# Performance work log

Hardware: AMD Instinct MI355X
Metric: run time of the kernel (lower is better)

Reference implementation:

```python
import jax, jax.numpy as jnp
import numpy as np

D_MODEL = 256
KSIZE = 16
EPS = 1e-5


def conv1d(x, w, b):
    # x: [B, C, N], w: [O, C, K], SAME padding over node axis
    y = jax.lax.conv_general_dilated(x, w, window_strides=(1,), padding='SAME',
                                     dimension_numbers=('NCH', 'OIH', 'NCH'))
    return y + b[None, :, None]


def layernorm(x, g, b):
    mu = jnp.mean(x, axis=-1, keepdims=True)
    var = jnp.mean(jnp.square(x - mu), axis=-1, keepdims=True)
    return (x - mu) * jax.lax.rsqrt(var + EPS) * g + b


def setup_inputs() -> dict:
    key = jax.random.key(0)
    ks = jax.random.split(key, 16)
    B, N, d, K = 4, 2048, D_MODEL, KSIZE
    conv_scale = 1.0 / np.sqrt(d * K)
    lin_scale = 1.0 / np.sqrt(d)
    return {
        'src': jax.random.normal(ks[0], (B, N, d), jnp.float32),
        'x_lst': jnp.zeros((B, N, N), jnp.float32),
        'adj': jax.random.randint(ks[1], (B, N, N), 0, 2, jnp.int32),
        'dis': jax.random.uniform(ks[2], (B, N, N), jnp.float32),
        'Wq': jax.random.normal(ks[3], (d, d, K), jnp.float32) * conv_scale,
        'bq': jnp.zeros((d,), jnp.float32),
        'Wk': jax.random.normal(ks[4], (d, d, K), jnp.float32) * conv_scale,
        'bk': jnp.zeros((d,), jnp.float32),
        'Wv': jax.random.normal(ks[5], (d, d, K), jnp.float32) * conv_scale,
        'bv': jnp.zeros((d,), jnp.float32),
        'W1': jax.random.normal(ks[6], (d, d), jnp.float32) * lin_scale,
        'b1': jnp.zeros((d,), jnp.float32),
        'W2': jax.random.normal(ks[7], (d, d), jnp.float32) * lin_scale,
        'b2': jnp.zeros((d,), jnp.float32),
        'W3': jax.random.normal(ks[8], (d, d), jnp.float32) * lin_scale,
        'b3': jnp.zeros((d,), jnp.float32),
        'g1': jnp.ones((d,), jnp.float32),
        'be1': jnp.zeros((d,), jnp.float32),
        'g2': jnp.ones((d,), jnp.float32),
        'be2': jnp.zeros((d,), jnp.float32),
    }


def reference(src, x_lst, adj, dis, Wq, bq, Wk, bk, Wv, bv,
              W1, b1, W2, b2, W3, b3, g1, be1, g2, be2):
    # ---- _ga_block: transpose to channel-major, graph attention ----
    x = jnp.swapaxes(src, -2, -1)                      # [B, d, N]
    q = conv1d(x, Wq, bq)                              # [B, d, N]
    k = conv1d(x, Wk, bk)
    v = conv1d(x, Wv, bv)
    scale = 1.0 / jnp.sqrt(jnp.asarray(D_MODEL, src.dtype))
    scores = jnp.einsum('bdn,bdm->bnm', q, k) * scale  # [B, N, N]
    scores = scores - dis                              # distance bias
    scores = jnp.where(adj > 0, scores, jnp.asarray(-1e9, scores.dtype))
    attn = jax.nn.softmax(scores, axis=-1)             # [B, N, N]
    x_lst_new = x_lst + attn                           # accumulated attention state
    out = jnp.einsum('bnm,bdm->bdn', attn, v)          # [B, d, N]
    x1 = jnp.swapaxes(out, -2, -1)                     # [B, N, d] (dropout = identity in eval)
    # ---- residual + norm1 ----
    h = layernorm(src + x1, g1, be1)
    # ---- 3-layer LeakyReLU MLP + residual + norm2 ----
    m = jax.nn.leaky_relu(h @ W1.T + b1)
    m = jax.nn.leaky_relu(m @ W2.T + b2)
    m = m @ W3.T + b3
    h = layernorm(h + m, g2, be2)
    return h, x_lst_new
```

## Files before the change

kernel.cpp:

```cpp
#include <hip/hip_runtime.h>
#include <stdint.h>

typedef _Float16 h16;
typedef _Float16 h4v __attribute__((ext_vector_type(4)));
typedef _Float16 h8v __attribute__((ext_vector_type(8)));
typedef float    f4v __attribute__((ext_vector_type(4)));
typedef int      i4v __attribute__((ext_vector_type(4)));

#define NBATCH 4
#define NNODE  2048
#define DM     256
#define NPAD   2063
#define QKELEM 2097152
#define PARTN  (8192 * 256)

__device__ __forceinline__ void async16(const void* g, void* l) {
#if __has_builtin(__builtin_amdgcn_global_load_lds)
  __builtin_amdgcn_global_load_lds((__attribute__((address_space(1))) void*)g,
                                   (__attribute__((address_space(3))) void*)l, 16, 0, 0);
#else
  *(f4v*)l = *(const f4v*)g;
#endif
}

#define BARRIER() do { asm volatile("" ::: "memory"); __builtin_amdgcn_s_barrier(); asm volatile("" ::: "memory"); } while (0)
#define MFMA16 __builtin_amdgcn_mfma_f32_16x16x32_f16

__device__ __forceinline__ void gemm_tile(
    const h16* Abase, int astride,
    const h16* Bbase, int bstride,
    h16* As, h16* Bs, f4v acc[4][4], int kiters)
{
  const int tid  = threadIdx.x;
  const int lane = tid & 63;
  const int wv   = tid >> 6;
  const int srow = tid >> 2;
  const int sch  = ((tid & 3) ^ ((tid >> 3) & 3)) * 8;
  const h16* gA0 = Abase + (long)srow * astride + sch;
  const h16* gA1 = Abase + (long)(srow + 64) * astride + sch;
  const h16* gB0 = Bbase + (long)srow * bstride + sch;
  const h16* gB1 = Bbase + (long)(srow + 64) * bstride + sch;
  h16* lA0 = As + tid * 8;
  h16* lA1 = As + 2048 + tid * 8;
  h16* lB0 = Bs + tid * 8;
  h16* lB1 = Bs + 2048 + tid * 8;
  const int swz = ((lane & 15) >> 1) & 3;
  const int qq  = ((lane >> 4) ^ swz) * 8;
  const int amr = ((wv & 1) * 64 + (lane & 15)) * 32 + qq;
  const int bnr = ((wv >> 1) * 64 + (lane & 15)) * 32 + qq;

  for (int kt = 0; kt < kiters; ++kt) {
    const int k0 = kt * 32;
    __syncthreads();
    async16(gA0 + k0, lA0);
    async16(gA1 + k0, lA1);
    async16(gB0 + k0, lB0);
    async16(gB1 + k0, lB1);
    asm volatile("s_waitcnt vmcnt(0)" ::: "memory");
    __syncthreads();
    h8v af[4], bf[4];
#pragma unroll
    for (int i = 0; i < 4; ++i) af[i] = *(const h8v*)(As + amr + i * 512);
#pragma unroll
    for (int j = 0; j < 4; ++j) bf[j] = *(const h8v*)(Bs + bnr + j * 512);
#pragma unroll
    for (int i = 0; i < 4; ++i)
#pragma unroll
      for (int j = 0; j < 4; ++j)
        acc[i][j] = MFMA16(af[i], bf[j], acc[i][j], 0, 0, 0);
  }
}

__device__ __forceinline__ void zero_acc(f4v acc[4][4]) {
#pragma unroll
  for (int i = 0; i < 4; ++i)
#pragma unroll
    for (int j = 0; j < 4; ++j) {
      f4v z = {0.f, 0.f, 0.f, 0.f};
      acc[i][j] = z;
    }
}

template<int ASTRIDE, int BSTRIDE>
__device__ __forceinline__ void gemm256_pipe(
    const h16* __restrict__ Abase, const h16* __restrict__ Bbase,
    h16* As, h16* Bs, f4v (&acc)[8][4], const int kiters)
{
  const int tid  = threadIdx.x;
  const int lane = tid & 63, wv = tid >> 6;

  const int rh = tid >> 3;
  const int cs = (((tid & 7) ^ ((tid >> 3) & 7)) << 3);
  const h16* AgT = Abase + (long)rh * ASTRIDE + cs;
  const h16* BgT = Bbase + (long)rh * BSTRIDE + cs;
  h16* lA = As + tid * 8;
  h16* lB = Bs + tid * 8;

  auto stageA = [&](int kt, int half) {
    h16* d = lA + ((kt & 1) << 14) + (half << 13);
    const h16* g = AgT + (long)half * 128 * ASTRIDE + kt * 64;
    async16(g, d);
    async16(g + 64 * ASTRIDE, d + 4096);
  };
  auto stageB = [&](int kt, int half) {
    h16* d = lB + ((kt & 1) << 14) + (half << 13);
    const h16* g = BgT + (long)half * 128 * BSTRIDE + kt * 64;
    async16(g, d);
    async16(g + 64 * BSTRIDE, d + 4096);
  };

  const int wr = wv >> 2, wc = wv & 3;
  const int e0 = (((lane >> 4) ^ (lane & 7)) << 3);
  const int e1 = e0 ^ 32;
  const h16* pA0 = As + (wr * 128 + (lane & 15)) * 64 + e0;
  const h16* pA1 = pA0 + (e1 - e0);
  const h16* pB0 = Bs + (wc * 64 + (lane & 15)) * 64 + e0;
  const h16* pB1 = pB0 + (e1 - e0);

#pragma unroll
  for (int i = 0; i < 8; ++i)
#pragma unroll
    for (int j = 0; j < 4; ++j) { f4v z = {0.f, 0.f, 0.f, 0.f}; acc[i][j] = z; }

  stageA(0, 0); stageA(0, 1); stageB(0, 0); stageB(0, 1); stageA(1, 0);
  asm volatile("s_waitcnt vmcnt(2)" ::: "memory");
  BARRIER();

#pragma unroll 1
  for (int kt = 0; kt < kiters; ++kt) {
    const int sb = (kt & 1) << 14;
    h8v ar[4][2], bL[2][2], bR[2][2];
#pragma unroll
    for (int i = 0; i < 4; ++i) {
      ar[i][0] = *(const h8v*)(pA0 + sb + i * 1024);
      ar[i][1] = *(const h8v*)(pA1 + sb + i * 1024);
    }
#pragma unroll
    for (int j = 0; j < 2; ++j) {
      bL[j][0] = *(const h8v*)(pB0 + sb + j * 1024);
      bL[j][1] = *(const h8v*)(pB1 + sb + j * 1024);
    }
    if (kt < kiters - 1) stageA(kt + 1, 1);
    BARRIER();
    __builtin_amdgcn_s_setprio(1);
#pragma unroll
    for (int i = 0; i < 4; ++i)
#pragma unroll
      for (int j = 0; j < 2; ++j) {
        acc[i][j] = MFMA16(ar[i][0], bL[j][0], acc[i][j], 0, 0, 0);
        acc[i][j] = MFMA16(ar[i][1], bL[j][1], acc[i][j], 0, 0, 0);
      }
    __builtin_amdgcn_s_setprio(0);
    BARRIER();
#pragma unroll
    for (int j = 0; j < 2; ++j) {
      bR[j][0] = *(const h8v*)(pB0 + sb + (j + 2) * 1024);
      bR[j][1] = *(const h8v*)(pB1 + sb + (j + 2) * 1024);
    }
    if (kt < kiters - 1) stageB(kt + 1, 0);
    BARRIER();
    __builtin_amdgcn_s_setprio(1);
#pragma unroll
    for (int i = 0; i < 4; ++i)
#pragma unroll
      for (int j = 0; j < 2; ++j) {
        acc[i][j + 2] = MFMA16(ar[i][0], bR[j][0], acc[i][j + 2], 0, 0, 0);
        acc[i][j + 2] = MFMA16(ar[i][1], bR[j][1], acc[i][j + 2], 0, 0, 0);
      }
    __builtin_amdgcn_s_setprio(0);
    BARRIER();
#pragma unroll
    for (int i = 0; i < 4; ++i) {
      ar[i][0] = *(const h8v*)(pA0 + sb + (i + 4) * 1024);
      ar[i][1] = *(const h8v*)(pA1 + sb + (i + 4) * 1024);
    }
    if (kt < kiters - 1) stageB(kt + 1, 1);
    BARRIER();
    __builtin_amdgcn_s_setprio(1);
#pragma unroll
    for (int i = 0; i < 4; ++i)
#pragma unroll
      for (int j = 0; j < 2; ++j) {
        acc[i + 4][j + 2] = MFMA16(ar[i][0], bR[j][0], acc[i + 4][j + 2], 0, 0, 0);
        acc[i + 4][j + 2] = MFMA16(ar[i][1], bR[j][1], acc[i + 4][j + 2], 0, 0, 0);
      }
    __builtin_amdgcn_s_setprio(0);
    BARRIER();
#pragma unroll
    for (int j = 0; j < 2; ++j) {
      bL[j][0] = *(const h8v*)(pB0 + sb + j * 1024);
      bL[j][1] = *(const h8v*)(pB1 + sb + j * 1024);
    }
    if (kt < kiters - 2) {
      stageA(kt + 2, 0);
      asm volatile("s_waitcnt vmcnt(2)" ::: "memory");
    } else if (kt == kiters - 2) {
      asm volatile("s_waitcnt vmcnt(0)" ::: "memory");
    }
    BARRIER();
    __builtin_amdgcn_s_setprio(1);
#pragma unroll
    for (int i = 0; i < 4; ++i)
#pragma unroll
      for (int j = 0; j < 2; ++j) {
        acc[i + 4][j] = MFMA16(ar[i][0], bL[j][0], acc[i + 4][j], 0, 0, 0);
        acc[i + 4][j] = MFMA16(ar[i][1], bL[j][1], acc[i + 4][j], 0, 0, 0);
      }
    __builtin_amdgcn_s_setprio(0);
    BARRIER();
  }
}

#define NSRC_BLK 8252
__global__ __launch_bounds__(256) void prep_all_kernel(
    const float* __restrict__ src,
    const float* __restrict__ Wq, const float* __restrict__ Wk, const float* __restrict__ Wv,
    const float* __restrict__ W1, const float* __restrict__ W2, const float* __restrict__ W3,
    h16* __restrict__ Xpad, h16* __restrict__ Wt, h16* __restrict__ Wl)
{
  __shared__ float plds[16][257];
  const int bi = blockIdx.x, tid = threadIdx.x;
  if (bi < NSRC_BLK) {
    int idx = bi * 256 + tid;
    int c = idx & 255;
    int row = idx >> 8;
    int b = row / NPAD;
    int n = row - b * NPAD;
    float v = 0.f;
    int ns = n - 7;
    if (ns >= 0 && ns < NNODE) v = src[((long)b * NNODE + ns) * DM + c];
    Xpad[idx] = (h16)v;
  } else if (bi < NSRC_BLK + 768) {
    const int q = bi - NSRC_BLK;
    const int w = q >> 8, o = q & 255;
    const float* W = (w == 0) ? Wq : (w == 1) ? Wk : Wv;
    const float* base = W + (long)o * 4096;
    f4v r0 = *(const f4v*)(base + tid * 16);
    f4v r1 = *(const f4v*)(base + tid * 16 + 4);
    f4v r2 = *(const f4v*)(base + tid * 16 + 8);
    f4v r3 = *(const f4v*)(base + tid * 16 + 12);
#pragma unroll
    for (int k = 0; k < 4; ++k) {
      plds[k][tid] = r0[k]; plds[4 + k][tid] = r1[k];
      plds[8 + k][tid] = r2[k]; plds[12 + k][tid] = r3[k];
    }
    __syncthreads();
    const int t = tid >> 4, c0 = (tid & 15) * 16;
    h16* out = Wt + ((long)(w * 256 + o)) * 4096 + t * 256 + c0;
    h8v o0, o1;
#pragma unroll
    for (int k = 0; k < 8; ++k) { o0[k] = (h16)plds[t][c0 + k]; o1[k] = (h16)plds[t][c0 + 8 + k]; }
    *(h8v*)out = o0;
    *(h8v*)(out + 8) = o1;
  } else {
    int idx = (bi - NSRC_BLK - 768) * 256 + tid;
    int w = idx >> 16;
    int rem = idx & 65535;
    const float* W = (w == 0) ? W1 : (w == 1) ? W2 : W3;
    Wl[idx] = (h16)W[rem];
  }
}

__global__ __launch_bounds__(512) void conv_gemm256_kernel(
    const h16* __restrict__ Xpad, const h16* __restrict__ Wt,
    h16* __restrict__ Qp, h16* __restrict__ Kp, h16* __restrict__ Vp)
{
  __shared__ __align__(16) h16 As[32768];
  __shared__ __align__(16) h16 Bs[32768];
  const int lane = threadIdx.x & 63, wv = threadIdx.x >> 6;
  const int mt = blockIdx.x, w = blockIdx.y, ks = blockIdx.z;
  const int m0 = mt * 256;
  const int b  = m0 >> 11, n0 = m0 & 2047;

  const h16* Abase = Xpad + ((long)(b * NPAD + n0) << 8) + ((long)ks << 11);
  const h16* Bbase = Wt + ((long)w << 20) + ((long)ks << 11);

  f4v acc[8][4];
  gemm256_pipe<256, 4096>(Abase, Bbase, As, Bs, acc, 32);

  h16* dst = ((w == 0) ? Qp : (w == 1) ? Kp : Vp) + (long)ks * QKELEM;
  const int wr = wv >> 2, wc = wv & 3;
  const int rb = (lane >> 4) * 4;
  const int cb = wc * 64 + (lane & 15);
  const int mrow0 = m0 + wr * 128;
#pragma unroll
  for (int i = 0; i < 8; ++i)
#pragma unroll
    for (int j = 0; j < 4; ++j) {
      const int gc = cb + j * 16;
#pragma unroll
      for (int e = 0; e < 4; ++e) {
        const int gr = mrow0 + i * 16 + rb + e;
        dst[(long)gr * 256 + gc] = (h16)acc[i][j][e];
      }
    }
}

__global__ __launch_bounds__(256) void conv_reduce_kernel(
    const h16* __restrict__ Qp, const h16* __restrict__ Kp, const h16* __restrict__ Vp,
    const float* __restrict__ bq, const float* __restrict__ bk, const float* __restrict__ bv,
    h16* __restrict__ Qb, h16* __restrict__ Kb, h16* __restrict__ Vt)
{
  __shared__ float T[64][65];
  const int bi = blockIdx.x, tid = threadIdx.x;
  if (bi < 2048) {
    const long gid = (long)bi * 256 + tid;
    const int which = gid >= (QKELEM / 8);
    const long e = (gid - (long)which * (QKELEM / 8)) * 8;
    const h16* P = which ? Kp : Qp;
    const float* bias = which ? bk : bq;
    h8v p0 = *(const h8v*)(P + e);
    h8v p1 = *(const h8v*)(P + QKELEM + e);
    const int c0 = (int)(e & 255);
    h8v o;
#pragma unroll
    for (int k = 0; k < 8; ++k) o[k] = (h16)((float)p0[k] + (float)p1[k] + bias[c0 + k]);
    *(h8v*)((which ? Kb : Qb) + e) = o;
  } else {
    const int q = bi - 2048;
    const int mt = q >> 2, ct = q & 3;
    const int m0 = mt * 64, c0 = ct * 64;
    const int b = m0 >> 11, n0 = m0 & 2047;
    const int rr = tid >> 3, cc = (tid & 7) * 8;
#pragma unroll
    for (int p = 0; p < 2; ++p) {
      const int r = p * 32 + rr;
      const long so = (long)(m0 + r) * 256 + c0 + cc;
      h8v p0 = *(const h8v*)(Vp + so);
      h8v p1 = *(const h8v*)(Vp + QKELEM + so);
#pragma unroll
      for (int e = 0; e < 8; ++e) T[r][cc + e] = (float)p0[e] + (float)p1[e];
    }
    __syncthreads();
#pragma unroll
    for (int p = 0; p < 2; ++p) {
      const int d = p * 32 + rr;
      const float bias_v = bv[c0 + d];
      h8v o;
#pragma unroll
      for (int e = 0; e < 8; ++e) o[e] = (h16)(T[cc + e][d] + bias_v);
      *(h8v*)(Vt + ((long)(b * 256 + c0 + d)) * 2048 + n0 + cc) = o;
    }
  }
}

#define MBS 144
__global__ __launch_bounds__(256) void scores_gemm_kernel(
    const h16* __restrict__ Q, const h16* __restrict__ Km,
    const float* __restrict__ dis, const int* __restrict__ adj,
    h16* __restrict__ Sh)
{
  __shared__ __align__(16) h16 As[4096];
  __shared__ __align__(16) h16 Bs[4096];
  __shared__ __align__(16) h16 Mb[128 * MBS];
  const int nt = blockIdx.x, mt = blockIdx.y, b = blockIdx.z;
  const int tid = threadIdx.x, lane = tid & 63, wv = tid >> 6;

  const h16* Abase = Q + ((long)b * NNODE + nt * 128) * 256;
  const h16* Bbase = Km + ((long)b * NNODE + mt * 128) * 256;

  const int srow = tid >> 2;
  const int sch  = ((tid & 3) ^ ((tid >> 3) & 3)) * 8;
  const h16* gA0 = Abase + (long)srow * 256 + sch;
  const h16* gA1 = Abase + (long)(srow + 64) * 256 + sch;
  const h16* gB0 = Bbase + (long)srow * 256 + sch;
  const h16* gB1 = Bbase + (long)(srow + 64) * 256 + sch;
  h16* lA0 = As + tid * 8;
  h16* lA1 = As + 2048 + tid * 8;
  h16* lB0 = Bs + tid * 8;
  h16* lB1 = Bs + 2048 + tid * 8;
  const int swz = ((lane & 15) >> 1) & 3;
  const int qq  = ((lane >> 4) ^ swz) * 8;
  const int amr = ((wv & 1) * 64 + (lane & 15)) * 32 + qq;
  const int bnr = ((wv >> 1) * 64 + (lane & 15)) * 32 + qq;

  const long gbase = (long)b * NNODE * NNODE + (long)(nt * 128) * 2048 + mt * 128;
  f4v acc[4][4];
  zero_acc(acc);

#pragma unroll 1
  for (int kt = 0; kt < 8; ++kt) {
    const int f0 = kt * 2048 + tid * 4;
    const int f1 = f0 + 1024;
    const int r0 = f0 >> 7, c0 = f0 & 127;
    const int r1 = f1 >> 7, c1 = f1 & 127;
    const long g0 = gbase + (long)r0 * 2048 + c0;
    const long g1 = gbase + (long)r1 * 2048 + c1;
    __syncthreads();
    f4v dv0 = *(const f4v*)(dis + g0);
    f4v dv1 = *(const f4v*)(dis + g1);
    i4v av0 = *(const i4v*)(adj + g0);
    i4v av1 = *(const i4v*)(adj + g1);
    const int k0 = kt * 32;
    async16(gA0 + k0, lA0);
    async16(gA1 + k0, lA1);
    async16(gB0 + k0, lB0);
    async16(gB1 + k0, lB1);
    asm volatile("s_waitcnt vmcnt(0)" ::: "memory");
    h4v m0, m1;
#pragma unroll
    for (int k = 0; k < 4; ++k) {
      m0[k] = (av0[k] > 0) ? (h16)(-dv0[k]) : (h16)(-30000.0f);
      m1[k] = (av1[k] > 0) ? (h16)(-dv1[k]) : (h16)(-30000.0f);
    }
    *(h4v*)(Mb + r0 * MBS + c0) = m0;
    *(h4v*)(Mb + r1 * MBS + c1) = m1;
    __syncthreads();
    h8v af[4], bf[4];
#pragma unroll
    for (int i = 0; i < 4; ++i) af[i] = *(const h8v*)(As + amr + i * 512);
#pragma unroll
    for (int j = 0; j < 4; ++j) bf[j] = *(const h8v*)(Bs + bnr + j * 512);
#pragma unroll
    for (int i = 0; i < 4; ++i)
#pragma unroll
      for (int j = 0; j < 4; ++j)
        acc[i][j] = MFMA16(af[i], bf[j], acc[i][j], 0, 0, 0);
  }

  const int rbase = (wv & 1) * 64 + (lane >> 4) * 4;
  const int cbase = (wv >> 1) * 64 + (lane & 15);
#pragma unroll
  for (int i = 0; i < 4; ++i) {
#pragma unroll
    for (int e = 0; e < 4; ++e) {
      const int row = rbase + i * 16 + e;
      const long ro = gbase + (long)row * 2048;
#pragma unroll
      for (int j = 0; j < 4; ++j) {
        const int col = cbase + j * 16;
        const float sv = acc[i][j][e] * 0.0625f + (float)Mb[row * MBS + col];
        Sh[ro + col] = (h16)sv;
      }
    }
  }
}

__global__ __launch_bounds__(256) void softmax_kernel(
    h16* __restrict__ Sh, const float* __restrict__ x_lst, float* __restrict__ out_x)
{
  const int r = blockIdx.x;
  const long ro = (long)r * 2048;
  const int tid = threadIdx.x, lane = tid & 63, wv = tid >> 6;
  const int j0 = tid * 4;
  __shared__ float wmax[4], wsum[4];

  h4v sv0 = *(const h4v*)(Sh + ro + j0);
  h4v sv1 = *(const h4v*)(Sh + ro + 1024 + j0);

  float s[8];
#pragma unroll
  for (int k = 0; k < 4; ++k) { s[k] = (float)sv0[k]; s[k + 4] = (float)sv1[k]; }

  float m = s[0];
#pragma unroll
  for (int k = 1; k < 8; ++k) m = fmaxf(m, s[k]);
#pragma unroll
  for (int off = 32; off > 0; off >>= 1) m = fmaxf(m, __shfl_xor(m, off, 64));
  if (lane == 0) wmax[wv] = m;
  __syncthreads();
  m = fmaxf(fmaxf(wmax[0], wmax[1]), fmaxf(wmax[2], wmax[3]));

  float p[8], ls = 0.f;
#pragma unroll
  for (int k = 0; k < 8; ++k) { p[k] = __expf(s[k] - m); ls += p[k]; }
#pragma unroll
  for (int off = 32; off > 0; off >>= 1) ls += __shfl_xor(ls, off, 64);
  if (lane == 0) wsum[wv] = ls;
  __syncthreads();
  const float inv = 1.0f / (wsum[0] + wsum[1] + wsum[2] + wsum[3]);

  f4v x0 = *(const f4v*)(x_lst + ro + j0);
  f4v x1 = *(const f4v*)(x_lst + ro + 1024 + j0);
  f4v o0, o1;
  h4v pv0, pv1;
#pragma unroll
  for (int k = 0; k < 4; ++k) {
    const float a = p[k] * inv, bq = p[k + 4] * inv;
    o0[k] = x0[k] + a; o1[k] = x1[k] + bq;
    pv0[k] = (h16)a; pv1[k] = (h16)bq;
  }
  *(f4v*)(out_x + ro + j0) = o0;
  *(f4v*)(out_x + ro + 1024 + j0) = o1;
  *(h4v*)(Sh + ro + j0) = pv0;
  *(h4v*)(Sh + ro + 1024 + j0) = pv1;
}

__global__ __launch_bounds__(256) void av_gemm_kernel(
    const h16* __restrict__ Attn, const h16* __restrict__ Vt, h16* __restrict__ X1p)
{
  __shared__ __align__(16) h16 As[4096];
  __shared__ __align__(16) h16 Bs[4096];
  const int nt = blockIdx.x, b = blockIdx.z;
  const int ct = blockIdx.y & 1, ks = blockIdx.y >> 1;
  const h16* Abase = Attn + ((long)b * NNODE + nt * 128) * 2048 + ks * 1024;
  const h16* Bbase = Vt + ((long)b * 256 + ct * 128) * 2048 + ks * 1024;
  f4v acc[4][4];
  zero_acc(acc);
  gemm_tile(Abase, 2048, Bbase, 2048, As, Bs, acc, 32);

  const int lane = threadIdx.x & 63, wv = threadIdx.x >> 6;
  const int rbase = (wv & 1) * 64 + (lane >> 4) * 4;
  const int cbase = (wv >> 1) * 64 + (lane & 15);
  h16* dst = X1p + (long)ks * PARTN;
#pragma unroll
  for (int i = 0; i < 4; ++i) {
#pragma unroll
    for (int e = 0; e < 4; ++e) {
      const long row = (long)b * NNODE + nt * 128 + rbase + i * 16 + e;
#pragma unroll
      for (int j = 0; j < 4; ++j) {
        const int col = ct * 128 + cbase + j * 16;
        dst[row * 256 + col] = (h16)acc[i][j][e];
      }
    }
  }
}

__device__ __forceinline__ float wred_sum(float v) {
#pragma unroll
  for (int off = 32; off > 0; off >>= 1) v += __shfl_xor(v, off, 64);
  return v;
}

__global__ __launch_bounds__(256) void ln1_kernel(
    const float* __restrict__ X, const h16* __restrict__ Y, const h16* __restrict__ Y2,
    const float* __restrict__ g, const float* __restrict__ bb,
    float* __restrict__ outF, h16* __restrict__ outH)
{
  const int wv = threadIdx.x >> 6, lane = threadIdx.x & 63;
  const long r = (long)blockIdx.x * 4 + wv;
  const long off = r * 256 + lane * 4;
  f4v x = *(const f4v*)(X + off);
  h4v y = *(const h4v*)(Y + off);
  h4v y2 = *(const h4v*)(Y2 + off);
  float v[4];
  float sum = 0.f, sq = 0.f;
#pragma unroll
  for (int k = 0; k < 4; ++k) {
    v[k] = x[k] + (float)y[k] + (float)y2[k];
    sum += v[k]; sq += v[k] * v[k];
  }
  sum = wred_sum(sum);
  sq  = wred_sum(sq);
  const float mu = sum * (1.0f / 256.0f);
  const float var = sq * (1.0f / 256.0f) - mu * mu;
  const float rs = rsqrtf(var + 1e-5f);
  f4v gg = *(const f4v*)(g + lane * 4);
  f4v be = *(const f4v*)(bb + lane * 4);
  f4v o;
#pragma unroll
  for (int k = 0; k < 4; ++k) o[k] = (v[k] - mu) * rs * gg[k] + be[k];
  *(f4v*)(outF + off) = o;
  h4v hv;
#pragma unroll
  for (int k = 0; k < 4; ++k) hv[k] = (h16)o[k];
  *(h4v*)(outH + off) = hv;
}

__global__ __launch_bounds__(256) void mlp_fused_kernel(
    const h16* __restrict__ H16, const float* __restrict__ Hf,
    const h16* __restrict__ Wl,
    const float* __restrict__ b1, const float* __restrict__ b2, const float* __restrict__ b3,
    const float* __restrict__ g2, const float* __restrict__ be2,
    float* __restrict__ out_h)
{
  __shared__ h16 Xa[32][264];
  __shared__ h16 Xb[32][264];
  __shared__ __align__(16) h16 Bs[8192];
  const int tid = threadIdx.x, lane = tid & 63, wv = tid >> 6;
  const int m0 = blockIdx.x * 32;

  {
    const int r = tid >> 3, cq = (tid & 7) * 32;
    const h16* s = H16 + (long)(m0 + r) * 256 + cq;
#pragma unroll
    for (int k = 0; k < 4; ++k)
      *(h8v*)&Xa[r][cq + k * 8] = *(const h8v*)(s + k * 8);
  }

  const int srow = tid >> 2;
  const int sch  = ((tid & 3) ^ ((tid >> 3) & 3)) * 8;
  h16* lB = Bs + tid * 8;
  const int quad = lane >> 4;
  const float* biases[3] = {b1, b2, b3};

  for (int layer = 0; layer < 3; ++layer) {
    const h16* W = Wl + layer * 65536;
    const h16 (*Xi)[264] = (layer == 1) ? (const h16(*)[264])Xb : (const h16(*)[264])Xa;
    h16 (*Xo)[264] = (layer == 1) ? Xa : Xb;
    f4v acc[2][4];
#pragma unroll
    for (int i = 0; i < 2; ++i)
#pragma unroll
      for (int j = 0; j < 4; ++j) { f4v z = {0.f,0.f,0.f,0.f}; acc[i][j] = z; }

    for (int kt = 0; kt < 8; ++kt) {
      __syncthreads();
      const h16* gB = W + (long)srow * 256 + kt * 32 + sch;
      async16(gB, lB);
      async16(gB + 64 * 256, lB + 64 * 32);
      async16(gB + 128 * 256, lB + 128 * 32);
      async16(gB + 192 * 256, lB + 192 * 32);
      asm volatile("s_waitcnt vmcnt(0)" ::: "memory");
      __syncthreads();
      h8v af[2], bf[4];
#pragma unroll
      for (int i = 0; i < 2; ++i)
        af[i] = *(const h8v*)&Xi[i * 16 + (lane & 15)][kt * 32 + quad * 8];
#pragma unroll
      for (int j = 0; j < 4; ++j) {
        const int n = wv * 64 + j * 16 + (lane & 15);
        const int q = (quad ^ ((n >> 1) & 3)) * 8;
        bf[j] = *(const h8v*)(Bs + n * 32 + q);
      }
#pragma unroll
      for (int i = 0; i < 2; ++i)
#pragma unroll
        for (int j = 0; j < 4; ++j)
          acc[i][j] = MFMA16(af[i], bf[j], acc[i][j], 0, 0, 0);
    }
    const int rb = quad * 4;
    const int cb = wv * 64 + (lane & 15);
    const float* bias = biases[layer];
    const bool leaky = (layer < 2);
#pragma unroll
    for (int j = 0; j < 4; ++j) {
      const int col = cb + j * 16;
      const float bv = bias[col];
#pragma unroll
      for (int i = 0; i < 2; ++i)
#pragma unroll
        for (int e = 0; e < 4; ++e) {
          float v = acc[i][j][e] + bv;
          if (leaky) v = (v >= 0.f) ? v : 0.01f * v;
          Xo[i * 16 + rb + e][col] = (h16)v;
        }
    }
  }
  __syncthreads();

  const int r = tid >> 3, c0 = (tid & 7) * 32;
  const float* hrow = Hf + (long)(m0 + r) * 256 + c0;
  float v[32];
  float s = 0.f, sq = 0.f;
#pragma unroll
  for (int k8 = 0; k8 < 8; ++k8) {
    f4v h4 = *(const f4v*)(hrow + k8 * 4);
#pragma unroll
    for (int e = 0; e < 4; ++e) {
      float t = (float)Xb[r][c0 + k8 * 4 + e] + h4[e];
      v[k8 * 4 + e] = t; s += t; sq += t * t;
    }
  }
#pragma unroll
  for (int off = 1; off < 8; off <<= 1) { s += __shfl_xor(s, off, 64); sq += __shfl_xor(sq, off, 64); }
  const float mu = s * (1.0f / 256.0f);
  const float var = sq * (1.0f / 256.0f) - mu * mu;
  const float rs = rsqrtf(var + 1e-5f);
  float* orow = out_h + (long)(m0 + r) * 256 + c0;
#pragma unroll
  for (int k8 = 0; k8 < 8; ++k8) {
    f4v gg = *(const f4v*)(g2 + c0 + k8 * 4);
    f4v be = *(const f4v*)(be2 + c0 + k8 * 4);
    f4v o;
#pragma unroll
    for (int e = 0; e < 4; ++e) o[e] = (v[k8 * 4 + e] - mu) * rs * gg[e] + be[e];
    *(f4v*)(orow + k8 * 4) = o;
  }
}

extern "C" void kernel_launch(void* const* d_in, const int* in_sizes, int n_in,
                              void* d_out, int out_size, void* d_ws, size_t ws_size,
                              hipStream_t stream)
{
  const float* src  = (const float*)d_in[0];
  const float* xlst = (const float*)d_in[1];
  const int*   adj  = (const int*)d_in[2];
  const float* dis  = (const float*)d_in[3];
  const float* Wq   = (const float*)d_in[4];
  const float* bq   = (const float*)d_in[5];
  const float* Wk   = (const float*)d_in[6];
  const float* bk   = (const float*)d_in[7];
  const float* Wv   = (const float*)d_in[8];
  const float* bvp  = (const float*)d_in[9];
  const float* W1   = (const float*)d_in[10];
  const float* b1   = (const float*)d_in[11];
  const float* W2   = (const float*)d_in[12];
  const float* b2   = (const float*)d_in[13];
  const float* W3   = (const float*)d_in[14];
  const float* b3   = (const float*)d_in[15];
  const float* g1   = (const float*)d_in[16];
  const float* be1  = (const float*)d_in[17];
  const float* g2   = (const float*)d_in[18];
  const float* be2  = (const float*)d_in[19];
  (void)in_sizes; (void)n_in; (void)out_size; (void)ws_size;

  char* ws = (char*)d_ws;
  size_t off = 0;
  auto alloc = [&](size_t bytes) -> void* {
    void* p = ws + off;
    off += (bytes + 1023) & ~(size_t)1023;
    return p;
  };
  h16*   Xpad = (h16*)  alloc((size_t)NBATCH * NPAD * DM * 2);
  h16*   Wt   = (h16*)  alloc((size_t)3 * 256 * 4096 * 2);
  h16*   Wl   = (h16*)  alloc((size_t)3 * 256 * 256 * 2);
  h16*   Qb   = (h16*)  alloc((size_t)QKELEM * 2);
  h16*   Kb   = (h16*)  alloc((size_t)QKELEM * 2);
  h16*   Vt   = (h16*)  alloc((size_t)QKELEM * 2);
  char*  R    = (char*) alloc((size_t)66000 * 1024);
  h16*   Qp   = (h16*)R;
  h16*   Kp   = (h16*)(R + (size_t)2 * QKELEM * 2);
  h16*   Vp   = (h16*)(R + (size_t)4 * QKELEM * 2);
  h16*   Sh   = (h16*)R;
  h16*   X1p  = (h16*)(R + (size_t)8 * QKELEM * 2);
  float* H    = (float*)(R + (size_t)12 * QKELEM * 2);
  h16*   H16  = (h16*)((char*)H + (size_t)PARTN * 4);

  float* out_h = (float*)d_out;
  float* out_x = out_h + (size_t)NBATCH * NNODE * DM;

  prep_all_kernel<<<NSRC_BLK + 768 + 768, 256, 0, stream>>>(
      src, Wq, Wk, Wv, W1, W2, W3, Xpad, Wt, Wl);
  conv_gemm256_kernel<<<dim3(32, 3, 2), 512, 0, stream>>>(Xpad, Wt, Qp, Kp, Vp);
  conv_reduce_kernel<<<2048 + 512, 256, 0, stream>>>(
      Qp, Kp, Vp, bq, bk, bvp, Qb, Kb, Vt);
  scores_gemm_kernel<<<dim3(16, 16, 4), 256, 0, stream>>>(Qb, Kb, dis, adj, Sh);
  softmax_kernel<<<NBATCH * NNODE, 256, 0, stream>>>(Sh, xlst, out_x);
  av_gemm_kernel<<<dim3(16, 4, 4), 256, 0, stream>>>(Sh, Vt, X1p);
  ln1_kernel<<<(NBATCH * NNODE) / 4, 256, 0, stream>>>(src, X1p, X1p + PARTN, g1, be1, H, H16);
  mlp_fused_kernel<<<NBATCH * NNODE / 32, 256, 0, stream>>>(
      H16, H, Wl, b1, b2, b3, g2, be2, out_h);
}
```

Measured before the change: 413.1 us.

## Replace split-K conv GEMM with full-K 128x192 tiles and fused bias epilogue

```diff
diff --git a/kernel.cpp b/kernel.cpp
--- a/kernel.cpp
+++ b/kernel.cpp
@@ -79,136 +79,6 @@
       f4v z = {0.f, 0.f, 0.f, 0.f};
       acc[i][j] = z;
     }
-}
-
-template<int ASTRIDE, int BSTRIDE>
-__device__ __forceinline__ void gemm256_pipe(
-    const h16* __restrict__ Abase, const h16* __restrict__ Bbase,
-    h16* As, h16* Bs, f4v (&acc)[8][4], const int kiters)
-{
-  const int tid  = threadIdx.x;
-  const int lane = tid & 63, wv = tid >> 6;
-
-  const int rh = tid >> 3;
-  const int cs = (((tid & 7) ^ ((tid >> 3) & 7)) << 3);
-  const h16* AgT = Abase + (long)rh * ASTRIDE + cs;
-  const h16* BgT = Bbase + (long)rh * BSTRIDE + cs;
-  h16* lA = As + tid * 8;
-  h16* lB = Bs + tid * 8;
-
-  auto stageA = [&](int kt, int half) {
-    h16* d = lA + ((kt & 1) << 14) + (half << 13);
-    const h16* g = AgT + (long)half * 128 * ASTRIDE + kt * 64;
-    async16(g, d);
-    async16(g + 64 * ASTRIDE, d + 4096);
-  };
-  auto stageB = [&](int kt, int half) {
-    h16* d = lB + ((kt & 1) << 14) + (half << 13);
-    const h16* g = BgT + (long)half * 128 * BSTRIDE + kt * 64;
-    async16(g, d);
-    async16(g + 64 * BSTRIDE, d + 4096);
-  };
-
-  const int wr = wv >> 2, wc = wv & 3;
-  const int e0 = (((lane >> 4) ^ (lane & 7)) << 3);
-  const int e1 = e0 ^ 32;
-  const h16* pA0 = As + (wr * 128 + (lane & 15)) * 64 + e0;
-  const h16* pA1 = pA0 + (e1 - e0);
-  const h16* pB0 = Bs + (wc * 64 + (lane & 15)) * 64 + e0;
-  const h16* pB1 = pB0 + (e1 - e0);
-
-#pragma unroll
-  for (int i = 0; i < 8; ++i)
-#pragma unroll
-    for (int j = 0; j < 4; ++j) { f4v z = {0.f, 0.f, 0.f, 0.f}; acc[i][j] = z; }
-
-  stageA(0, 0); stageA(0, 1); stageB(0, 0); stageB(0, 1); stageA(1, 0);
-  asm volatile("s_waitcnt vmcnt(2)" ::: "memory");
-  BARRIER();
-
-#pragma unroll 1
-  for (int kt = 0; kt < kiters; ++kt) {
-    const int sb = (kt & 1) << 14;
-    h8v ar[4][2], bL[2][2], bR[2][2];
-#pragma unroll
-    for (int i = 0; i < 4; ++i) {
-      ar[i][0] = *(const h8v*)(pA0 + sb + i * 1024);
-      ar[i][1] = *(const h8v*)(pA1 + sb + i * 1024);
-    }
-#pragma unroll
-    for (int j = 0; j < 2; ++j) {
-      bL[j][0] = *(const h8v*)(pB0 + sb + j * 1024);
-      bL[j][1] = *(const h8v*)(pB1 + sb + j * 1024);
-    }
-    if (kt < kiters - 1) stageA(kt + 1, 1);
-    BARRIER();
-    __builtin_amdgcn_s_setprio(1);
-#pragma unroll
-    for (int i = 0; i < 4; ++i)
-#pragma unroll
-      for (int j = 0; j < 2; ++j) {
-        acc[i][j] = MFMA16(ar[i][0], bL[j][0], acc[i][j], 0, 0, 0);
-        acc[i][j] = MFMA16(ar[i][1], bL[j][1], acc[i][j], 0, 0, 0);
-      }
-    __builtin_amdgcn_s_setprio(0);
-    BARRIER();
-#pragma unroll
-    for (int j = 0; j < 2; ++j) {
-      bR[j][0] = *(const h8v*)(pB0 + sb + (j + 2) * 1024);
-      bR[j][1] = *(const h8v*)(pB1 + sb + (j + 2) * 1024);
-    }
-    if (kt < kiters - 1) stageB(kt + 1, 0);
-    BARRIER();
-    __builtin_amdgcn_s_setprio(1);
-#pragma unroll
-    for (int i = 0; i < 4; ++i)
-#pragma unroll
-      for (int j = 0; j < 2; ++j) {
-        acc[i][j + 2] = MFMA16(ar[i][0], bR[j][0], acc[i][j + 2], 0, 0, 0);
-        acc[i][j + 2] = MFMA16(ar[i][1], bR[j][1], acc[i][j + 2], 0, 0, 0);
-      }
-    __builtin_amdgcn_s_setprio(0);
-    BARRIER();
-#pragma unroll
-    for (int i = 0; i < 4; ++i) {
-      ar[i][0] = *(const h8v*)(pA0 + sb + (i + 4) * 1024);
-      ar[i][1] = *(const h8v*)(pA1 + sb + (i + 4) * 1024);
-    }
-    if (kt < kiters - 1) stageB(kt + 1, 1);
-    BARRIER();
-    __builtin_amdgcn_s_setprio(1);
-#pragma unroll
-    for (int i = 0; i < 4; ++i)
-#pragma unroll
-      for (int j = 0; j < 2; ++j) {
-        acc[i + 4][j + 2] = MFMA16(ar[i][0], bR[j][0], acc[i + 4][j + 2], 0, 0, 0);
-        acc[i + 4][j + 2] = MFMA16(ar[i][1], bR[j][1], acc[i + 4][j + 2], 0, 0, 0);
-      }
-    __builtin_amdgcn_s_setprio(0);
-    BARRIER();
-#pragma unroll
-    for (int j = 0; j < 2; ++j) {
-      bL[j][0] = *(const h8v*)(pB0 + sb + j * 1024);
-      bL[j][1] = *(const h8v*)(pB1 + sb + j * 1024);
-    }
-    if (kt < kiters - 2) {
-      stageA(kt + 2, 0);
-      asm volatile("s_waitcnt vmcnt(2)" ::: "memory");
-    } else if (kt == kiters - 2) {
-      asm volatile("s_waitcnt vmcnt(0)" ::: "memory");
-    }
-    BARRIER();
-    __builtin_amdgcn_s_setprio(1);
-#pragma unroll
-    for (int i = 0; i < 4; ++i)
-#pragma unroll
-      for (int j = 0; j < 2; ++j) {
-        acc[i + 4][j] = MFMA16(ar[i][0], bL[j][0], acc[i + 4][j], 0, 0, 0);
-        acc[i + 4][j] = MFMA16(ar[i][1], bL[j][1], acc[i + 4][j], 0, 0, 0);
-      }
-    __builtin_amdgcn_s_setprio(0);
-    BARRIER();
-  }
 }
 
 #define NSRC_BLK 8252
@@ -261,86 +131,139 @@
   }
 }
 
-__global__ __launch_bounds__(512) void conv_gemm256_kernel(
+__global__ __launch_bounds__(512) void conv_gemm_full(
     const h16* __restrict__ Xpad, const h16* __restrict__ Wt,
-    h16* __restrict__ Qp, h16* __restrict__ Kp, h16* __restrict__ Vp)
-{
-  __shared__ __align__(16) h16 As[32768];
-  __shared__ __align__(16) h16 Bs[32768];
-  const int lane = threadIdx.x & 63, wv = threadIdx.x >> 6;
-  const int mt = blockIdx.x, w = blockIdx.y, ks = blockIdx.z;
-  const int m0 = mt * 256;
-  const int b  = m0 >> 11, n0 = m0 & 2047;
-
-  const h16* Abase = Xpad + ((long)(b * NPAD + n0) << 8) + ((long)ks << 11);
-  const h16* Bbase = Wt + ((long)w << 20) + ((long)ks << 11);
-
-  f4v acc[8][4];
-  gemm256_pipe<256, 4096>(Abase, Bbase, As, Bs, acc, 32);
-
-  h16* dst = ((w == 0) ? Qp : (w == 1) ? Kp : Vp) + (long)ks * QKELEM;
+    const float* __restrict__ bq, const float* __restrict__ bk, const float* __restrict__ bv,
+    h16* __restrict__ Qb, h16* __restrict__ Kb, h16* __restrict__ Vp)
+{
+  __shared__ __align__(16) h16 As[16384];
+  __shared__ __align__(16) h16 Bs[24576];
+  const int tid = threadIdx.x, lane = tid & 63, wv = tid >> 6;
+  const int mt = blockIdx.x, nt = blockIdx.y;
+  const int m0 = mt * 128;
+  const int b = m0 >> 11, n0 = m0 & 2047;
+
+  const int rh = tid >> 3;
+  const int cs = (((tid & 7) ^ ((tid >> 3) & 7)) << 3);
+  const h16* AgT = Xpad + ((long)(b * NPAD + n0) << 8) + (long)rh * 256 + cs;
+  const h16* BgT = Wt + (long)(nt * 192) * 4096 + (long)rh * 4096 + cs;
+  h16* lA = As + tid * 8;
+  h16* lB = Bs + tid * 8;
+
+  auto stageA = [&](int kt, int half) {
+    async16(AgT + (long)half * (64 * 256) + kt * 64,
+            lA + ((kt & 1) << 13) + (half << 12));
+  };
+  auto stageB = [&](int kt, int third) {
+    async16(BgT + (long)third * (64 * 4096) + kt * 64,
+            lB + (kt & 1) * 12288 + third * 4096);
+  };
+
   const int wr = wv >> 2, wc = wv & 3;
-  const int rb = (lane >> 4) * 4;
-  const int cb = wc * 64 + (lane & 15);
-  const int mrow0 = m0 + wr * 128;
-#pragma unroll
-  for (int i = 0; i < 8; ++i)
-#pragma unroll
-    for (int j = 0; j < 4; ++j) {
-      const int gc = cb + j * 16;
+  const int e0 = (((lane >> 4) ^ (lane & 7)) << 3);
+  const int e1 = e0 ^ 32;
+  const h16* pA0 = As + (wr * 64 + (lane & 15)) * 64 + e0;
+  const h16* pA1 = As + (wr * 64 + (lane & 15)) * 64 + e1;
+  const h16* pB0 = Bs + (wc * 48 + (lane & 15)) * 64 + e0;
+  const h16* pB1 = Bs + (wc * 48 + (lane & 15)) * 64 + e1;
+
+  f4v acc[4][3];
+#pragma unroll
+  for (int i = 0; i < 4; ++i)
+#pragma unroll
+    for (int j = 0; j < 3; ++j) { f4v z = {0.f, 0.f, 0.f, 0.f}; acc[i][j] = z; }
+
+  stageA(0, 0); stageA(0, 1); stageB(0, 0); stageB(0, 1); stageB(0, 2); stageA(1, 0);
+  asm volatile("s_waitcnt vmcnt(1)" ::: "memory");
+  BARRIER();
+
+#pragma unroll 1
+  for (int kt = 0; kt < 64; ++kt) {
+    const int sa = (kt & 1) << 13;
+    const int sb = (kt & 1) * 12288;
+    h8v a0[4], a1[4], bL[2][2], b2[2];
+#pragma unroll
+    for (int i = 0; i < 4; ++i) {
+      a0[i] = *(const h8v*)(pA0 + sa + i * 1024);
+      a1[i] = *(const h8v*)(pA1 + sa + i * 1024);
+    }
+#pragma unroll
+    for (int j = 0; j < 2; ++j) {
+      bL[j][0] = *(const h8v*)(pB0 + sb + j * 1024);
+      bL[j][1] = *(const h8v*)(pB1 + sb + j * 1024);
+    }
+    if (kt < 63) stageA(kt + 1, 1);
+    BARRIER();
+    __builtin_amdgcn_s_setprio(1);
+#pragma unroll
+    for (int i = 0; i < 4; ++i)
+#pragma unroll
+      for (int j = 0; j < 2; ++j) {
+        acc[i][j] = MFMA16(a0[i], bL[j][0], acc[i][j], 0, 0, 0);
+        acc[i][j] = MFMA16(a1[i], bL[j][1], acc[i][j], 0, 0, 0);
+      }
+    __builtin_amdgcn_s_setprio(0);
+    BARRIER();
+    b2[0] = *(const h8v*)(pB0 + sb + 2 * 1024);
+    b2[1] = *(const h8v*)(pB1 + sb + 2 * 1024);
+    if (kt < 63) { stageB(kt + 1, 0); stageB(kt + 1, 1); stageB(kt + 1, 2); }
+    if (kt < 62) {
+      stageA(kt + 2, 0);
+      asm volatile("s_waitcnt vmcnt(1)" ::: "memory");
+    } else if (kt == 62) {
+      asm volatile("s_waitcnt vmcnt(0)" ::: "memory");
+    }
+    BARRIER();
+    __builtin_amdgcn_s_setprio(1);
+#pragma unroll
+    for (int i = 0; i < 4; ++i) {
+      acc[i][2] = MFMA16(a0[i], b2[0], acc[i][2], 0, 0, 0);
+      acc[i][2] = MFMA16(a1[i], b2[1], acc[i][2], 0, 0, 0);
+    }
+    __builtin_amdgcn_s_setprio(0);
+    BARRIER();
+  }
+
+  const int rbase = (lane >> 4) * 4;
+  const int cIn = lane & 15;
+#pragma unroll
+  for (int j = 0; j < 3; ++j) {
+    const int gc = nt * 192 + wc * 48 + j * 16 + cIn;
+    const int w = gc >> 8, c = gc & 255;
+    const float bb = (w == 0) ? bq[c] : (w == 1) ? bk[c] : bv[c];
+    h16* dst = (w == 0) ? Qb : (w == 1) ? Kb : Vp;
+#pragma unroll
+    for (int i = 0; i < 4; ++i)
 #pragma unroll
       for (int e = 0; e < 4; ++e) {
-        const int gr = mrow0 + i * 16 + rb + e;
-        dst[(long)gr * 256 + gc] = (h16)acc[i][j][e];
+        const int row = m0 + wr * 64 + i * 16 + rbase + e;
+        dst[(long)row * 256 + c] = (h16)(acc[i][j][e] + bb);
       }
-    }
-}
-
-__global__ __launch_bounds__(256) void conv_reduce_kernel(
-    const h16* __restrict__ Qp, const h16* __restrict__ Kp, const h16* __restrict__ Vp,
-    const float* __restrict__ bq, const float* __restrict__ bk, const float* __restrict__ bv,
-    h16* __restrict__ Qb, h16* __restrict__ Kb, h16* __restrict__ Vt)
-{
-  __shared__ float T[64][65];
+  }
+}
+
+__global__ __launch_bounds__(256) void vt_kernel(
+    const h16* __restrict__ Vp, h16* __restrict__ Vt)
+{
+  __shared__ h16 T[64][72];
   const int bi = blockIdx.x, tid = threadIdx.x;
-  if (bi < 2048) {
-    const long gid = (long)bi * 256 + tid;
-    const int which = gid >= (QKELEM / 8);
-    const long e = (gid - (long)which * (QKELEM / 8)) * 8;
-    const h16* P = which ? Kp : Qp;
-    const float* bias = which ? bk : bq;
-    h8v p0 = *(const h8v*)(P + e);
-    h8v p1 = *(const h8v*)(P + QKELEM + e);
-    const int c0 = (int)(e & 255);
+  const int mt = bi >> 2, ct = bi & 3;
+  const int m0 = mt * 64, c0 = ct * 64;
+  const int b = m0 >> 11, n0 = m0 & 2047;
+  const int rr = tid >> 3, cc = (tid & 7) * 8;
+#pragma unroll
+  for (int p = 0; p < 2; ++p) {
+    const int r = p * 32 + rr;
+    *(h8v*)&T[r][cc] = *(const h8v*)(Vp + (long)(m0 + r) * 256 + c0 + cc);
+  }
+  __syncthreads();
+#pragma unroll
+  for (int p = 0; p < 2; ++p) {
+    const int d = p * 32 + rr;
     h8v o;
 #pragma unroll
-    for (int k = 0; k < 8; ++k) o[k] = (h16)((float)p0[k] + (float)p1[k] + bias[c0 + k]);
-    *(h8v*)((which ? Kb : Qb) + e) = o;
-  } else {
-    const int q = bi - 2048;
-    const int mt = q >> 2, ct = q & 3;
-    const int m0 = mt * 64, c0 = ct * 64;
-    const int b = m0 >> 11, n0 = m0 & 2047;
-    const int rr = tid >> 3, cc = (tid & 7) * 8;
-#pragma unroll
-    for (int p = 0; p < 2; ++p) {
-      const int r = p * 32 + rr;
-      const long so = (long)(m0 + r) * 256 + c0 + cc;
-      h8v p0 = *(const h8v*)(Vp + so);
-      h8v p1 = *(const h8v*)(Vp + QKELEM + so);
-#pragma unroll
-      for (int e = 0; e < 8; ++e) T[r][cc + e] = (float)p0[e] + (float)p1[e];
-    }
-    __syncthreads();
-#pragma unroll
-    for (int p = 0; p < 2; ++p) {
-      const int d = p * 32 + rr;
-      const float bias_v = bv[c0 + d];
-      h8v o;
-#pragma unroll
-      for (int e = 0; e < 8; ++e) o[e] = (h16)(T[cc + e][d] + bias_v);
-      *(h8v*)(Vt + ((long)(b * 256 + c0 + d)) * 2048 + n0 + cc) = o;
-    }
+    for (int e = 0; e < 8; ++e) o[e] = T[cc + e][d];
+    *(h8v*)(Vt + ((long)(b * 256 + c0 + d)) * 2048 + n0 + cc) = o;
   }
 }
 
@@ -710,9 +633,7 @@
   h16*   Kb   = (h16*)  alloc((size_t)QKELEM * 2);
   h16*   Vt   = (h16*)  alloc((size_t)QKELEM * 2);
   char*  R    = (char*) alloc((size_t)66000 * 1024);
-  h16*   Qp   = (h16*)R;
-  h16*   Kp   = (h16*)(R + (size_t)2 * QKELEM * 2);
-  h16*   Vp   = (h16*)(R + (size_t)4 * QKELEM * 2);
+  h16*   Vp   = (h16*)R;
   h16*   Sh   = (h16*)R;
   h16*   X1p  = (h16*)(R + (size_t)8 * QKELEM * 2);
   float* H    = (float*)(R + (size_t)12 * QKELEM * 2);
@@ -723,9 +644,9 @@
 
   prep_all_kernel<<<NSRC_BLK + 768 + 768, 256, 0, stream>>>(
       src, Wq, Wk, Wv, W1, W2, W3, Xpad, Wt, Wl);
-  conv_gemm256_kernel<<<dim3(32, 3, 2), 512, 0, stream>>>(Xpad, Wt, Qp, Kp, Vp);
-  conv_reduce_kernel<<<2048 + 512, 256, 0, stream>>>(
-      Qp, Kp, Vp, bq, bk, bvp, Qb, Kb, Vt);
+  conv_gemm_full<<<dim3(64, 4), 512, 0, stream>>>(
+      Xpad, Wt, bq, bk, bvp, Qb, Kb, Vp);
+  vt_kernel<<<512, 256, 0, stream>>>(Vp, Vt);
   scores_gemm_kernel<<<dim3(16, 16, 4), 256, 0, stream>>>(Qb, Kb, dis, adj, Sh);
   softmax_kernel<<<NBATCH * NNODE, 256, 0, stream>>>(Sh, xlst, out_x);
   av_gemm_kernel<<<dim3(16, 4, 4), 256, 0, stream>>>(Sh, Vt, X1p);
```

Result: slower. 429.6 us (+4.0%).
